# Kernel tuning notes

Measured on AMD Instinct MI355X. Metric: run time of the kernel, lower is better.

Reference implementation:

```python
import jax, jax.numpy as jnp
import numpy as np

N_NODES = 100000
N_EDGES = 800000
NODE_F = 32
EDGE_F = 16
HID = 128
EPS = 1e-5


def _bn(h, g, b):
    # BatchNorm1d in training mode: biased batch stats over dim 0
    m = h.mean(axis=0)
    v = jnp.mean((h - m) ** 2, axis=0)
    return (h - m) * jax.lax.rsqrt(v + EPS) * g + b


def _sage(x, src, dst, Wl, bl, Wr):
    # PyG SAGEConv (mean aggr): lin_l(mean_{j->i} x_j) + lin_r(x_i)
    s = jax.ops.segment_sum(x[src], dst, num_segments=N_NODES)
    cnt = jax.ops.segment_sum(jnp.ones((src.shape[0], 1), x.dtype), dst, num_segments=N_NODES)
    mean = s / jnp.maximum(cnt, 1.0)
    return mean @ Wl + bl + x @ Wr


def setup_inputs() -> dict:
    key = jax.random.key(0)
    ks = jax.random.split(key, 32)

    def lin(k, fi, fo):
        return jax.random.normal(k, (fi, fo), jnp.float32) / np.sqrt(fi)

    inp = {
        'x': jax.random.normal(ks[0], (N_NODES, NODE_F), jnp.float32),
        'edge_index': jax.random.randint(ks[1], (2, N_EDGES), 0, N_NODES),
        'edge_attr': jax.random.normal(ks[2], (N_EDGES, EDGE_F), jnp.float32),
        'edge_source': jax.random.randint(ks[3], (N_EDGES,), 0, N_NODES),
        'edge_target': jax.random.randint(ks[4], (N_EDGES,), 0, N_NODES),
        'W1l': lin(ks[5], NODE_F, HID), 'b1': jnp.zeros((HID,), jnp.float32), 'W1r': lin(ks[6], NODE_F, HID),
        'W2l': lin(ks[7], HID, HID), 'b2': jnp.zeros((HID,), jnp.float32), 'W2r': lin(ks[8], HID, HID),
        'bn1_g': jnp.ones((HID,), jnp.float32), 'bn1_b': jnp.zeros((HID,), jnp.float32),
        'bn2_g': jnp.ones((HID,), jnp.float32), 'bn2_b': jnp.zeros((HID,), jnp.float32),
        'We': lin(ks[9], EDGE_F, HID), 'be': jnp.zeros((HID,), jnp.float32),
        'bne_g': jnp.ones((HID,), jnp.float32), 'bne_b': jnp.zeros((HID,), jnp.float32),
        'Wm1': lin(ks[10], 3 * HID, HID), 'bm1': jnp.zeros((HID,), jnp.float32),
        'bnm_g': jnp.ones((HID,), jnp.float32), 'bnm_b': jnp.zeros((HID,), jnp.float32),
        'Wm2': lin(ks[11], HID, HID // 2), 'bm2': jnp.zeros((HID // 2,), jnp.float32),
        'Wm3': lin(ks[12], HID // 2, 1), 'bm3': jnp.zeros((1,), jnp.float32),
    }
    return inp


def reference(x, edge_index, edge_attr, edge_source, edge_target,
              W1l, b1, W1r, W2l, b2, W2r, bn1_g, bn1_b, bn2_g, bn2_b,
              We, be, bne_g, bne_b, Wm1, bm1, bnm_g, bnm_b, Wm2, bm2, Wm3, bm3):
    src, dst = edge_index[0], edge_index[1]
    h = jax.nn.relu(_bn(_sage(x, src, dst, W1l, b1, W1r), bn1_g, bn1_b))  # dropout = identity (eval)
    h = jax.nn.relu(_bn(_sage(h, src, dst, W2l, b2, W2r), bn2_g, bn2_b))
    ef = _bn(jax.nn.relu(edge_attr @ We + be), bne_g, bne_b)  # Linear->ReLU->BN->Dropout(id)
    z = jnp.concatenate([h[edge_source], h[edge_target], ef], axis=1)  # [E, 3*HID]
    z = _bn(jax.nn.relu(z @ Wm1 + bm1), bnm_g, bnm_b)
    z = jax.nn.relu(z @ Wm2 + bm2)
    return (z @ Wm3 + bm3).squeeze(-1)
```

## Files before the change

kernel.cpp:

```cpp
#include <hip/hip_runtime.h>
#include <hip/hip_bf16.h>

#define NN 100000
#define NE 800000
#define SCAN_NB 98

typedef __attribute__((ext_vector_type(8))) short bf16x8;
typedef __attribute__((ext_vector_type(4))) float f32x4;

__device__ __forceinline__ short f2b(float f) {
    unsigned u = __float_as_uint(f);
    unsigned r = (u + 0x7fffu + ((u >> 16) & 1u)) >> 16;
    return (short)r;
}
__device__ __forceinline__ float b2f(short s) {
    return __uint_as_float(((unsigned)(unsigned short)s) << 16);
}

__global__ __launch_bounds__(256) void k_hist(const int* __restrict__ ei, int* __restrict__ deg)
{
    int e = blockIdx.x * 256 + threadIdx.x;
    if (e < NE) atomicAdd(&deg[ei[NE + e]], 1);
}

__global__ __launch_bounds__(1024) void k_scan_a(const int* __restrict__ deg,
    int* __restrict__ tmp, int* __restrict__ bsum)
{
    __shared__ int sh[1024];
    int t = threadIdx.x, b = blockIdx.x;
    int idx = b * 1024 + t;
    int v = (idx < NN) ? deg[idx] : 0;
    sh[t] = v;
    __syncthreads();
    for (int ofs = 1; ofs < 1024; ofs <<= 1) {
        int u = (t >= ofs) ? sh[t - ofs] : 0;
        __syncthreads();
        sh[t] += u;
        __syncthreads();
    }
    if (idx < NN) tmp[idx] = sh[t] - v;
    if (t == 1023) bsum[b] = sh[1023];
}

__global__ void k_scan_b(const int* __restrict__ bsum, int* __restrict__ boff,
    int* __restrict__ rowptr)
{
    if (threadIdx.x == 0) {
        int acc = 0;
        for (int i = 0; i < SCAN_NB; i++) { boff[i] = acc; acc += bsum[i]; }
        rowptr[NN] = acc;
    }
}

__global__ __launch_bounds__(1024) void k_scan_c(const int* __restrict__ tmp,
    const int* __restrict__ boff, int* __restrict__ rowptr, int* __restrict__ wp)
{
    int b = blockIdx.x, t = threadIdx.x;
    int idx = b * 1024 + t;
    if (idx < NN) {
        int v = boff[b] + tmp[idx];
        rowptr[idx] = v; wp[idx] = v;
    }
}

__global__ __launch_bounds__(256) void k_scatter(const int* __restrict__ ei,
    int* __restrict__ wp, int* __restrict__ elist)
{
    int e = blockIdx.x * 256 + threadIdx.x;
    if (e < NE) {
        int d = ei[NE + e];
        int pos = atomicAdd(&wp[d], 1);
        elist[pos] = ei[e];
    }
}

__global__ __launch_bounds__(256) void k_gagg1(const float* __restrict__ x,
    const int* __restrict__ rowptr, const int* __restrict__ elist, float* __restrict__ meanX)
{
    int n = blockIdx.x * 8 + (threadIdx.x >> 5);
    int j = threadIdx.x & 31;
    int b = rowptr[n], e = rowptr[n + 1];
    float acc = 0.f;
    for (int i = b; i < e; i++) {
        int s = elist[i];
        acc += x[(size_t)s * 32 + j];
    }
    float inv = (e > b) ? 1.0f / (float)(e - b) : 1.0f;
    meanX[(size_t)n * 32 + j] = acc * inv;
}

__global__ __launch_bounds__(256) void k_gagg2(const short* __restrict__ h1b,
    const int* __restrict__ rowptr, const int* __restrict__ elist,
    const float* __restrict__ sc1, const float* __restrict__ sh1, short* __restrict__ m2b)
{
    int n = blockIdx.x * 8 + (threadIdx.x >> 5);
    int c0 = (threadIdx.x & 31) * 4;
    float sc[4], sh[4];
    #pragma unroll
    for (int i = 0; i < 4; i++) { sc[i] = sc1[c0 + i]; sh[i] = sh1[c0 + i]; }
    int b = rowptr[n], e = rowptr[n + 1];
    float acc[4] = {0.f, 0.f, 0.f, 0.f};
    for (int i = b; i < e; i++) {
        int s = elist[i];
        ushort4 u = *(const ushort4*)(h1b + (size_t)s * 128 + c0);
        acc[0] += fmaxf(b2f((short)u.x) * sc[0] + sh[0], 0.f);
        acc[1] += fmaxf(b2f((short)u.y) * sc[1] + sh[1], 0.f);
        acc[2] += fmaxf(b2f((short)u.z) * sc[2] + sh[2], 0.f);
        acc[3] += fmaxf(b2f((short)u.w) * sc[3] + sh[3], 0.f);
    }
    float inv = (e > b) ? 1.0f / (float)(e - b) : 1.0f;
    ushort4 o;
    o.x = (unsigned short)f2b(acc[0] * inv);
    o.y = (unsigned short)f2b(acc[1] * inv);
    o.z = (unsigned short)f2b(acc[2] * inv);
    o.w = (unsigned short)f2b(acc[3] * inv);
    *(ushort4*)(m2b + (size_t)n * 128 + c0) = o;
}

__global__ __launch_bounds__(256) void k_node_l1(
    const float* __restrict__ meanX, const float* __restrict__ x,
    const float* __restrict__ Wl, const float* __restrict__ Wr,
    const float* __restrict__ bias,
    short* __restrict__ outp, float* __restrict__ ssum, float* __restrict__ ssq)
{
    __shared__ __align__(16) float sWl[32][128];
    __shared__ __align__(16) float sWr[32][128];
    __shared__ __align__(16) float sA[32][36];
    __shared__ __align__(16) float sB[32][36];
    __shared__ float red[2][128], red2[2][128];
    int tid = threadIdx.x;
    int j = tid & 127, rg = tid >> 7;
    int r0 = blockIdx.x * 32;

    for (int f = tid * 4; f < 4096; f += 1024) {
        *(float4*)((float*)sWl + f) = *(const float4*)(Wl + f);
        *(float4*)((float*)sWr + f) = *(const float4*)(Wr + f);
    }
    {
        int r = tid >> 3, c = (tid & 7) * 4;
        *(float4*)(&sA[r][c]) = *(const float4*)(meanX + (size_t)(r0 + r) * 32 + c);
        *(float4*)(&sB[r][c]) = *(const float4*)(x + (size_t)(r0 + r) * 32 + c);
    }
    __syncthreads();

    float acc[16];
    #pragma unroll
    for (int r = 0; r < 16; r++) acc[r] = 0.0f;
    int rb = rg * 16;
    #pragma unroll
    for (int kq = 0; kq < 8; kq++) {
        int k = kq * 4;
        float wl0 = sWl[k][j], wl1 = sWl[k+1][j], wl2 = sWl[k+2][j], wl3 = sWl[k+3][j];
        float wr0 = sWr[k][j], wr1 = sWr[k+1][j], wr2 = sWr[k+2][j], wr3 = sWr[k+3][j];
        #pragma unroll
        for (int r = 0; r < 16; r++) {
            float4 a = *(float4*)(&sA[rb + r][k]);
            float4 b = *(float4*)(&sB[rb + r][k]);
            acc[r] += a.x*wl0 + a.y*wl1 + a.z*wl2 + a.w*wl3
                    + b.x*wr0 + b.y*wr1 + b.z*wr2 + b.w*wr3;
        }
    }
    float bj = bias[j];
    float s1 = 0.0f, s2 = 0.0f;
    #pragma unroll
    for (int r = 0; r < 16; r++) {
        float v = acc[r] + bj;
        outp[(size_t)(r0 + rb + r) * 128 + j] = f2b(v);
        s1 += v; s2 += v * v;
    }
    red[rg][j] = s1; red2[rg][j] = s2;
    __syncthreads();
    if (rg == 0) {
        atomicAdd(&ssum[j], red[0][j] + red[1][j]);
        atomicAdd(&ssq[j],  red2[0][j] + red2[1][j]);
    }
}

__global__ __launch_bounds__(256) void k_node_l2m(
    const short* __restrict__ m2b, const short* __restrict__ h1b,
    const float* __restrict__ sc1, const float* __restrict__ sh1,
    const short* __restrict__ W2cT, const float* __restrict__ bias,
    short* __restrict__ h2b, float* __restrict__ ssum, float* __restrict__ ssq)
{
    __shared__ __align__(16) short sK[32][264];
    __shared__ float sRed[2][128];
    __shared__ float sS[128], sH[128];
    const int tid = threadIdx.x;
    const int wave = tid >> 6, lane = tid & 63, quad = lane >> 4, ln = lane & 15;
    const int waveM = wave >> 1, waveN = wave & 1;
    const int colbase = 64 * waveN, row16 = 16 * waveM;
    if (tid < 128) { sS[tid] = sc1[tid]; sH[tid] = sh1[tid]; sRed[0][tid] = 0.f; sRed[1][tid] = 0.f; }

    bf16x8 bW[4][8];
    #pragma unroll
    for (int nt = 0; nt < 4; nt++)
        #pragma unroll
        for (int kk = 0; kk < 8; kk++)
            bW[nt][kk] = *(const bf16x8*)(W2cT + (size_t)(colbase + nt * 16 + ln) * 256 + kk * 32 + quad * 8);
    float bc[4];
    #pragma unroll
    for (int nt = 0; nt < 4; nt++) bc[nt] = bias[colbase + nt * 16 + ln];

    float s1[4] = {0,0,0,0}, s2[4] = {0,0,0,0};
    f32x4 zero = {0.f, 0.f, 0.f, 0.f};
    __syncthreads();

    for (int t = blockIdx.x; t < NN / 32; t += gridDim.x) {
        int r0 = t * 32;
        __syncthreads();
        {
            int r = tid >> 3, seg = tid & 7;
            if (seg < 4) {
                const bf16x8* src = (const bf16x8*)(m2b + (size_t)(r0 + r) * 128 + seg * 32);
                bf16x8* dst = (bf16x8*)(&sK[r][seg * 32]);
                dst[0] = src[0]; dst[1] = src[1]; dst[2] = src[2]; dst[3] = src[3];
            } else {
                int c0 = (seg - 4) * 32;
                const short* src = h1b + (size_t)(r0 + r) * 128 + c0;
                short tmp[32];
                #pragma unroll
                for (int i = 0; i < 32; i++)
                    tmp[i] = f2b(fmaxf(b2f(src[i]) * sS[c0 + i] + sH[c0 + i], 0.f));
                bf16x8* dst = (bf16x8*)(&sK[r][128 + c0]);
                dst[0] = *(bf16x8*)(tmp); dst[1] = *(bf16x8*)(tmp + 8);
                dst[2] = *(bf16x8*)(tmp + 16); dst[3] = *(bf16x8*)(tmp + 24);
            }
        }
        __syncthreads();
        f32x4 acc[4] = {zero, zero, zero, zero};
        #pragma unroll
        for (int kk = 0; kk < 8; kk++) {
            bf16x8 a = *(const bf16x8*)(&sK[row16 + ln][kk * 32 + quad * 8]);
            #pragma unroll
            for (int nt = 0; nt < 4; nt++)
                acc[nt] = __builtin_amdgcn_mfma_f32_16x16x32_bf16(a, bW[nt][kk], acc[nt], 0, 0, 0);
        }
        #pragma unroll
        for (int nt = 0; nt < 4; nt++) {
            int col = colbase + nt * 16 + ln;
            #pragma unroll
            for (int r = 0; r < 4; r++) {
                float v = acc[nt][r] + bc[nt];
                h2b[(size_t)(r0 + row16 + quad * 4 + r) * 128 + col] = f2b(v);
                s1[nt] += v; s2[nt] += v * v;
            }
        }
    }
    #pragma unroll
    for (int nt = 0; nt < 4; nt++) {
        float a1 = s1[nt], a2 = s2[nt];
        a1 += __shfl_down(a1, 32); a1 += __shfl_down(a1, 16);
        a2 += __shfl_down(a2, 32); a2 += __shfl_down(a2, 16);
        if (quad == 0) {
            atomicAdd(&sRed[0][colbase + nt * 16 + ln], a1);
            atomicAdd(&sRed[1][colbase + nt * 16 + ln], a2);
        }
    }
    __syncthreads();
    if (tid < 128) {
        atomicAdd(&ssum[tid], sRed[0][tid]);
        atomicAdd(&ssq[tid],  sRed[1][tid]);
    }
}

__global__ void k_bn_fin(const float* __restrict__ ssum, const float* __restrict__ ssq,
    const float* __restrict__ g, const float* __restrict__ b, float count,
    float* __restrict__ scale, float* __restrict__ shift)
{
    int j = threadIdx.x;
    float m = ssum[j] / count;
    float var = ssq[j] / count - m * m;
    float rs = rsqrtf(var + 1e-5f);
    float sc = g[j] * rs;
    scale[j] = sc;
    shift[j] = b[j] - m * sc;
}

__global__ void k_prep(const float* __restrict__ We, const float* __restrict__ Wm1,
                       const float* __restrict__ W2l, const float* __restrict__ W2r,
                       short* __restrict__ WteT, short* __restrict__ WmsT,
                       short* __restrict__ WmdT, short* __restrict__ W2cT)
{
    int j = threadIdx.x;
    int b = blockIdx.x;
    if (b == 0) {
        for (int k = 0; k < 32; k++)
            WteT[j * 32 + k] = (k < 16) ? f2b(We[k * 128 + j]) : (short)0;
    } else if (b == 1) {
        for (int k = 0; k < 128; k++) WmsT[j * 128 + k] = f2b(Wm1[k * 128 + j]);
    } else if (b == 2) {
        for (int k = 0; k < 128; k++) WmdT[j * 128 + k] = f2b(Wm1[(128 + k) * 128 + j]);
    } else if (b == 3) {
        for (int k = 0; k < 128; k++) W2cT[j * 256 + k] = f2b(W2l[k * 128 + j]);
    } else {
        for (int k = 0; k < 128; k++) W2cT[j * 256 + 128 + k] = f2b(W2r[k * 128 + j]);
    }
}

__global__ void k_fold_e(const float* __restrict__ ssum, const float* __restrict__ ssq,
    const float* __restrict__ g, const float* __restrict__ b,
    const float* __restrict__ Wm1, const float* __restrict__ bm1,
    short* __restrict__ W1pT, float* __restrict__ bm1p)
{
    __shared__ float sa[128], sc[128];
    int tid = threadIdx.x;
    float m = ssum[tid] / (float)NE;
    float var = ssq[tid] / (float)NE - m * m;
    float rs = rsqrtf(var + 1e-5f);
    float a = g[tid] * rs;
    sa[tid] = a; sc[tid] = b[tid] - m * a;
    __syncthreads();
    float acc = bm1[tid];
    for (int k = 0; k < 128; k++) {
        float w = Wm1[(256 + k) * 128 + tid];
        W1pT[tid * 128 + k] = f2b(sa[k] * w);
        acc += sc[k] * w;
    }
    bm1p[tid] = acc;
}

__global__ void k_fold_m(const float* __restrict__ ssum, const float* __restrict__ ssq,
    const float* __restrict__ g, const float* __restrict__ b,
    const float* __restrict__ Wm2, const float* __restrict__ bm2,
    short* __restrict__ W2pT, float* __restrict__ b2p)
{
    __shared__ float sa[128], sc[128];
    int tid = threadIdx.x;
    float m = ssum[tid] / (float)NE;
    float var = ssq[tid] / (float)NE - m * m;
    float rs = rsqrtf(var + 1e-5f);
    float a = g[tid] * rs;
    sa[tid] = a; sc[tid] = b[tid] - m * a;
    __syncthreads();
    if (tid < 64) {
        float acc = bm2[tid];
        for (int k = 0; k < 128; k++) {
            float w = Wm2[k * 64 + tid];
            W2pT[tid * 128 + k] = f2b(sa[k] * w);
            acc += sc[k] * w;
        }
        b2p[tid] = acc;
    }
}

__global__ __launch_bounds__(256) void k_proj_mfma(
    const short* __restrict__ h2b, const float* __restrict__ sc2, const float* __restrict__ sh2,
    const short* __restrict__ WT, short* __restrict__ C)
{
    __shared__ __align__(16) short sA[32][136];
    __shared__ float sS[128], sH[128];
    const int tid = threadIdx.x;
    const int wave = tid >> 6, lane = tid & 63, quad = lane >> 4, ln = lane & 15;
    const int waveM = wave >> 1, waveN = wave & 1;
    const int colbase = 64 * waveN, row16 = 16 * waveM;
    if (tid < 128) { sS[tid] = sc2[tid]; sH[tid] = sh2[tid]; }
    bf16x8 bW[4][4];
    #pragma unroll
    for (int nt = 0; nt < 4; nt++)
        #pragma unroll
        for (int kk = 0; kk < 4; kk++)
            bW[nt][kk] = *(const bf16x8*)(WT + (colbase + nt * 16 + ln) * 128 + kk * 32 + quad * 8);
    f32x4 zero = {0.f, 0.f, 0.f, 0.f};
    __syncthreads();
    for (int t = blockIdx.x; t < NN / 32; t += gridDim.x) {
        int r0 = t * 32;
        __syncthreads();
        {
            int r = tid >> 3, c0 = (tid & 7) * 16;
            const short* p = h2b + (size_t)(r0 + r) * 128 + c0;
            short tmp[16];
            #pragma unroll
            for (int i = 0; i < 16; i++)
                tmp[i] = f2b(fmaxf(b2f(p[i]) * sS[c0 + i] + sH[c0 + i], 0.f));
            *(bf16x8*)(&sA[r][c0])     = *(bf16x8*)tmp;
            *(bf16x8*)(&sA[r][c0 + 8]) = *(bf16x8*)(tmp + 8);
        }
        __syncthreads();
        f32x4 acc[4] = {zero, zero, zero, zero};
        #pragma unroll
        for (int kk = 0; kk < 4; kk++) {
            bf16x8 a = *(const bf16x8*)(&sA[row16 + ln][kk * 32 + quad * 8]);
            #pragma unroll
            for (int nt = 0; nt < 4; nt++)
                acc[nt] = __builtin_amdgcn_mfma_f32_16x16x32_bf16(a, bW[nt][kk], acc[nt], 0, 0, 0);
        }
        #pragma unroll
        for (int nt = 0; nt < 4; nt++) {
            int col = colbase + nt * 16 + ln;
            #pragma unroll
            for (int r = 0; r < 4; r++)
                C[(size_t)(r0 + row16 + quad * 4 + r) * 128 + col] = f2b(acc[nt][r]);
        }
    }
}

template<int MODE, bool STOREV = false>
__global__ __launch_bounds__(256) void k_edge_mfma(
    const float* __restrict__ ea,
    const short* __restrict__ WteT, const float* __restrict__ be,
    const short* __restrict__ W1pT, const float* __restrict__ bm1p,
    const short* __restrict__ hs, const short* __restrict__ hd,
    const int* __restrict__ esrc, const int* __restrict__ etgt,
    const short* __restrict__ W2pT, const float* __restrict__ b2p,
    const float* __restrict__ Wm3, const float* __restrict__ bm3,
    float* __restrict__ ssum, float* __restrict__ ssq,
    short* __restrict__ vbuf, float* __restrict__ outp)
{
    __shared__ __align__(16) short sT[32][136];
    __shared__ float sRed[2][128];
    __shared__ __align__(16) short sW2[64][136];
    __shared__ float sZ[32][69];
    __shared__ float sW3[64];

    const int tid = threadIdx.x;
    const int wave = tid >> 6, lane = tid & 63;
    const int quad = lane >> 4, ln = lane & 15;
    const int waveM = wave >> 1, waveN = wave & 1;
    const int colbase = 64 * waveN, row16 = 16 * waveM;

    if (MODE < 2) {
        if (tid < 128) { sRed[0][tid] = 0.f; sRed[1][tid] = 0.f; }
    }
    if (MODE >= 2) {
        int q = tid >> 2, kb = (tid & 3) * 32;
        const bf16x8* src = (const bf16x8*)(W2pT + q * 128 + kb);
        bf16x8* dst = (bf16x8*)(&sW2[q][kb]);
        dst[0] = src[0]; dst[1] = src[1]; dst[2] = src[2]; dst[3] = src[3];
        if (tid < 64) sW3[tid] = Wm3[tid];
    }

    bf16x8 bWe[4], bW1[4][4];
    if (MODE <= 2) {
        #pragma unroll
        for (int nt = 0; nt < 4; nt++) {
            bWe[nt] = *(const bf16x8*)(WteT + (colbase + nt * 16 + ln) * 32 + quad * 8);
            if (MODE >= 1) {
                #pragma unroll
                for (int kk = 0; kk < 4; kk++)
                    bW1[nt][kk] = *(const bf16x8*)(W1pT + (colbase + nt * 16 + ln) * 128 + kk * 32 + quad * 8);
            }
        }
    }
    float bec[4], bmc[4];
    #pragma unroll
    for (int nt = 0; nt < 4; nt++) {
        bec[nt] = (MODE <= 2) ? be[colbase + nt * 16 + ln] : 0.f;
        bmc[nt] = (MODE == 1 || MODE == 2) ? bm1p[colbase + nt * 16 + ln] : 0.f;
    }
    float b2c[2] = {0.f, 0.f};
    if (MODE >= 2) { b2c[0] = b2p[32 * waveN + ln]; b2c[1] = b2p[32 * waveN + 16 + ln]; }
    float bm3v = (MODE >= 2) ? bm3[0] : 0.f;

    float s1[4] = {0,0,0,0}, s2[4] = {0,0,0,0};
    f32x4 zero = {0.f, 0.f, 0.f, 0.f};
    __syncthreads();

    for (int t = blockIdx.x; t < NE / 32; t += gridDim.x) {
        const int e0 = t * 32;

        if (MODE == 3) {
            f32x4 vacc[2] = {zero, zero};
            #pragma unroll
            for (int kk = 0; kk < 4; kk++) {
                bf16x8 aV = *(const bf16x8*)(vbuf + (size_t)(e0 + row16 + ln) * 128 + kk * 32 + quad * 8);
                #pragma unroll
                for (int n2 = 0; n2 < 2; n2++) {
                    bf16x8 bV = *(const bf16x8*)(&sW2[32 * waveN + n2 * 16 + ln][kk * 32 + quad * 8]);
                    vacc[n2] = __builtin_amdgcn_mfma_f32_16x16x32_bf16(aV, bV, vacc[n2], 0, 0, 0);
                }
            }
            __syncthreads();
            #pragma unroll
            for (int n2 = 0; n2 < 2; n2++) {
                int col2 = 32 * waveN + n2 * 16 + ln;
                #pragma unroll
                for (int r = 0; r < 4; r++)
                    sZ[row16 + quad * 4 + r][col2] = fmaxf(vacc[n2][r] + b2c[n2], 0.f);
            }
            __syncthreads();
            if (wave == 0) {
                int rw = lane & 31, half = lane >> 5;
                float o = 0.f;
                #pragma unroll 8
                for (int k2 = 0; k2 < 32; k2++)
                    o += sZ[rw][half * 32 + k2] * sW3[half * 32 + k2];
                o += __shfl_down(o, 32);
                if (lane < 32) outp[e0 + rw] = o + bm3v;
            }
            continue;
        }

        bf16x8 aE;
        #pragma unroll
        for (int i = 0; i < 8; i++) aE[i] = 0;
        if (quad < 2) {
            const float* p = ea + (size_t)(e0 + row16 + ln) * 16 + quad * 8;
            float4 f0 = *(const float4*)p, f1 = *(const float4*)(p + 4);
            aE[0]=f2b(f0.x); aE[1]=f2b(f0.y); aE[2]=f2b(f0.z); aE[3]=f2b(f0.w);
            aE[4]=f2b(f1.x); aE[5]=f2b(f1.y); aE[6]=f2b(f1.z); aE[7]=f2b(f1.w);
        }
        f32x4 tacc[4];
        #pragma unroll
        for (int nt = 0; nt < 4; nt++)
            tacc[nt] = __builtin_amdgcn_mfma_f32_16x16x32_bf16(aE, bWe[nt], zero, 0, 0, 0);

        if (MODE == 0) {
            #pragma unroll
            for (int nt = 0; nt < 4; nt++)
                #pragma unroll
                for (int r = 0; r < 4; r++) {
                    float v = fmaxf(tacc[nt][r] + bec[nt], 0.f);
                    s1[nt] += v; s2[nt] += v * v;
                }
            continue;
        }

        __syncthreads();
        #pragma unroll
        for (int nt = 0; nt < 4; nt++) {
            int col = colbase + nt * 16 + ln;
            #pragma unroll
            for (int r = 0; r < 4; r++)
                sT[row16 + quad * 4 + r][col] = f2b(fmaxf(tacc[nt][r] + bec[nt], 0.f));
        }
        __syncthreads();

        f32x4 uacc[4] = {zero, zero, zero, zero};
        #pragma unroll
        for (int kk = 0; kk < 4; kk++) {
            bf16x8 aU = *(const bf16x8*)(&sT[row16 + ln][kk * 32 + quad * 8]);
            #pragma unroll
            for (int nt = 0; nt < 4; nt++)
                uacc[nt] = __builtin_amdgcn_mfma_f32_16x16x32_bf16(aU, bW1[nt][kk], uacc[nt], 0, 0, 0);
        }

        int4 is4 = *(const int4*)(esrc + e0 + row16 + quad * 4);
        int4 it4 = *(const int4*)(etgt + e0 + row16 + quad * 4);
        int isv[4] = {is4.x, is4.y, is4.z, is4.w};
        int itv[4] = {it4.x, it4.y, it4.z, it4.w};

        if (MODE == 1) {
            #pragma unroll
            for (int nt = 0; nt < 4; nt++) {
                int col = colbase + nt * 16 + ln;
                #pragma unroll
                for (int r = 0; r < 4; r++) {
                    float v = uacc[nt][r] + bmc[nt]
                            + b2f(hs[(size_t)isv[r] * 128 + col]) + b2f(hd[(size_t)itv[r] * 128 + col]);
                    v = fmaxf(v, 0.f);
                    s1[nt] += v; s2[nt] += v * v;
                    if constexpr (STOREV)
                        vbuf[(size_t)(e0 + row16 + quad * 4 + r) * 128 + col] = f2b(v);
                }
            }
        } else {
            __syncthreads();
            #pragma unroll
            for (int nt = 0; nt < 4; nt++) {
                int col = colbase + nt * 16 + ln;
                #pragma unroll
                for (int r = 0; r < 4; r++) {
                    float v = uacc[nt][r] + bmc[nt]
                            + b2f(hs[(size_t)isv[r] * 128 + col]) + b2f(hd[(size_t)itv[r] * 128 + col]);
                    sT[row16 + quad * 4 + r][col] = f2b(fmaxf(v, 0.f));
                }
            }
            __syncthreads();
            f32x4 vacc[2] = {zero, zero};
            #pragma unroll
            for (int kk = 0; kk < 4; kk++) {
                bf16x8 aV = *(const bf16x8*)(&sT[row16 + ln][kk * 32 + quad * 8]);
                #pragma unroll
                for (int n2 = 0; n2 < 2; n2++) {
                    bf16x8 bV = *(const bf16x8*)(&sW2[32 * waveN + n2 * 16 + ln][kk * 32 + quad * 8]);
                    vacc[n2] = __builtin_amdgcn_mfma_f32_16x16x32_bf16(aV, bV, vacc[n2], 0, 0, 0);
                }
            }
            #pragma unroll
            for (int n2 = 0; n2 < 2; n2++) {
                int col2 = 32 * waveN + n2 * 16 + ln;
                #pragma unroll
                for (int r = 0; r < 4; r++)
                    sZ[row16 + quad * 4 + r][col2] = fmaxf(vacc[n2][r] + b2c[n2], 0.f);
            }
            __syncthreads();
            if (wave == 0) {
                int rw = lane & 31, half = lane >> 5;
                float o = 0.f;
                #pragma unroll 8
                for (int k2 = 0; k2 < 32; k2++)
                    o += sZ[rw][half * 32 + k2] * sW3[half * 32 + k2];
                o += __shfl_down(o, 32);
                if (lane < 32) outp[e0 + rw] = o + bm3v;
            }
        }
    }

    if (MODE < 2) {
        #pragma unroll
        for (int nt = 0; nt < 4; nt++) {
            float a1 = s1[nt], a2 = s2[nt];
            a1 += __shfl_down(a1, 32); a1 += __shfl_down(a1, 16);
            a2 += __shfl_down(a2, 32); a2 += __shfl_down(a2, 16);
            if (quad == 0) {
                atomicAdd(&sRed[0][colbase + nt * 16 + ln], a1);
                atomicAdd(&sRed[1][colbase + nt * 16 + ln], a2);
            }
        }
        __syncthreads();
        if (tid < 128) {
            atomicAdd(&ssum[tid], sRed[0][tid]);
            atomicAdd(&ssq[tid],  sRed[1][tid]);
        }
    }
}

extern "C" void kernel_launch(void* const* d_in, const int* in_sizes, int n_in,
                              void* d_out, int out_size, void* d_ws, size_t ws_size,
                              hipStream_t stream) {
    const float* x     = (const float*)d_in[0];
    const int*   ei    = (const int*)  d_in[1];
    const float* eattr = (const float*)d_in[2];
    const int*   esrc  = (const int*)  d_in[3];
    const int*   etgt  = (const int*)  d_in[4];
    const float* W1l = (const float*)d_in[5];  const float* b1 = (const float*)d_in[6];
    const float* W1r = (const float*)d_in[7];
    const float* W2l = (const float*)d_in[8];  const float* b2 = (const float*)d_in[9];
    const float* W2r = (const float*)d_in[10];
    const float* bn1_g = (const float*)d_in[11]; const float* bn1_b = (const float*)d_in[12];
    const float* bn2_g = (const float*)d_in[13]; const float* bn2_b = (const float*)d_in[14];
    const float* We  = (const float*)d_in[15]; const float* be  = (const float*)d_in[16];
    const float* bne_g = (const float*)d_in[17]; const float* bne_b = (const float*)d_in[18];
    const float* Wm1 = (const float*)d_in[19]; const float* bm1 = (const float*)d_in[20];
    const float* bnm_g = (const float*)d_in[21]; const float* bnm_b = (const float*)d_in[22];
    const float* Wm2 = (const float*)d_in[23]; const float* bm2 = (const float*)d_in[24];
    const float* Wm3 = (const float*)d_in[25]; const float* bm3 = (const float*)d_in[26];
    float* out = (float*)d_out;

    char* base = (char*)d_ws;
    size_t o = 0;
    auto A = [&](size_t bytes) { char* p = base + o; o = (o + bytes + 255) & ~(size_t)255; return p; };
    short* hsb   = (short*)A((size_t)NN * 128 * 2);
    short* hdb   = (short*)A((size_t)NN * 128 * 2);
    int*   deg   = (int*)  A((size_t)NN * 4);
    int*   rowptr= (int*)  A((size_t)(NN + 1) * 4);
    int*   wp    = (int*)  A((size_t)NN * 4);
    int*   elist = (int*)  A((size_t)NE * 4);
    float* st    = (float*)A(1024 * 4);
    int*   bsum  = (int*)  A(SCAN_NB * 4);
    int*   boff  = (int*)  A(SCAN_NB * 4);
    float* sc1   = (float*)A(512); float* sh1 = (float*)A(512);
    float* sc2   = (float*)A(512); float* sh2 = (float*)A(512);
    float* bm1p  = (float*)A(512); float* b2p = (float*)A(256);
    short* WteT  = (short*)A(128 * 32 * 2);
    short* W1pT  = (short*)A(128 * 128 * 2);
    short* WmsT  = (short*)A(128 * 128 * 2);
    short* WmdT  = (short*)A(128 * 128 * 2);
    short* W2pT  = (short*)A(64 * 128 * 2);
    short* W2cT  = (short*)A(128 * 256 * 2);
    size_t chain = o;
    float* meanX = (float*)A((size_t)NN * 32 * 4);
    short* h1b   = (short*)A((size_t)NN * 128 * 2);
    short* m2b   = (short*)A((size_t)NN * 128 * 2);
    short* h2b   = (short*)A((size_t)NN * 128 * 2);
    int*   stmp  = (int*)meanX;
    short* vbuf  = (short*)(base + chain);
    bool storev = ws_size >= chain + (size_t)NE * 128 * 2;

    hipMemsetAsync(deg, 0, (size_t)NN * 4, stream);
    hipMemsetAsync(st, 0, 1024 * 4, stream);

    k_prep<<<5, 128, 0, stream>>>(We, Wm1, W2l, W2r, WteT, WmsT, WmdT, W2cT);
    k_hist<<<(NE + 255) / 256, 256, 0, stream>>>(ei, deg);
    k_scan_a<<<SCAN_NB, 1024, 0, stream>>>(deg, stmp, bsum);
    k_scan_b<<<1, 64, 0, stream>>>(bsum, boff, rowptr);
    k_scan_c<<<SCAN_NB, 1024, 0, stream>>>(stmp, boff, rowptr, wp);
    k_scatter<<<(NE + 255) / 256, 256, 0, stream>>>(ei, wp, elist);

    k_edge_mfma<0><<<1024, 256, 0, stream>>>(eattr, WteT, be, W1pT, bm1p, hsb, hdb,
        esrc, etgt, W2pT, b2p, Wm3, bm3, st + 512, st + 640, nullptr, out);
    k_fold_e<<<1, 128, 0, stream>>>(st + 512, st + 640, bne_g, bne_b, Wm1, bm1, W1pT, bm1p);

    k_gagg1<<<NN / 8, 256, 0, stream>>>(x, rowptr, elist, meanX);
    k_node_l1<<<NN / 32, 256, 0, stream>>>(meanX, x, W1l, W1r, b1, h1b, st + 0, st + 128);
    k_bn_fin<<<1, 128, 0, stream>>>(st + 0, st + 128, bn1_g, bn1_b, (float)NN, sc1, sh1);

    k_gagg2<<<NN / 8, 256, 0, stream>>>(h1b, rowptr, elist, sc1, sh1, m2b);
    k_node_l2m<<<640, 256, 0, stream>>>(m2b, h1b, sc1, sh1, W2cT, b2, h2b, st + 256, st + 384);
    k_bn_fin<<<1, 128, 0, stream>>>(st + 256, st + 384, bn2_g, bn2_b, (float)NN, sc2, sh2);

    k_proj_mfma<<<640, 256, 0, stream>>>(h2b, sc2, sh2, WmsT, hsb);
    k_proj_mfma<<<640, 256, 0, stream>>>(h2b, sc2, sh2, WmdT, hdb);

    if (storev)
        k_edge_mfma<1, true><<<1280, 256, 0, stream>>>(eattr, WteT, be, W1pT, bm1p, hsb, hdb,
            esrc, etgt, W2pT, b2p, Wm3, bm3, st + 768, st + 896, vbuf, out);
    else
        k_edge_mfma<1, false><<<1280, 256, 0, stream>>>(eattr, WteT, be, W1pT, bm1p, hsb, hdb,
            esrc, etgt, W2pT, b2p, Wm3, bm3, st + 768, st + 896, nullptr, out);
    k_fold_m<<<1, 128, 0, stream>>>(st + 768, st + 896, bnm_g, bnm_b, Wm2, bm2, W2pT, b2p);

    if (storev)
        k_edge_mfma<3><<<2048, 256, 0, stream>>>(eattr, WteT, be, W1pT, bm1p, hsb, hdb,
            esrc, etgt, W2pT, b2p, Wm3, bm3, nullptr, nullptr, vbuf, out);
    else
        k_edge_mfma<2><<<1280, 256, 0, stream>>>(eattr, WteT, be, W1pT, bm1p, hsb, hdb,
            esrc, etgt, W2pT, b2p, Wm3, bm3, nullptr, nullptr, nullptr, out);
}
```

Measured before the change: 864.4 us.

## Coalesce edge gathers via shared staging, merge proj launches, parallelize final dot

Edge kernels now gather the hs[src] and hd[tgt] rows with 16-byte vector loads per thread, issued before the MFMA. The summed values are staged in a new shared fp32 tile, replacing scattered per-element bf16 gathers in the epilogue. The two projection launches are merged into one 1280-block launch, and the final 64-wide dot product is spread across all four waves with xor shuffles instead of one wave. Launch bounds request 5 blocks per CU, which may pressure registers, and the added shared tile raises LDS use per block.

```diff
diff --git a/kernel.cpp b/kernel.cpp
--- a/kernel.cpp
+++ b/kernel.cpp
@@ -345,7 +345,8 @@
 
 __global__ __launch_bounds__(256) void k_proj_mfma(
     const short* __restrict__ h2b, const float* __restrict__ sc2, const float* __restrict__ sh2,
-    const short* __restrict__ WT, short* __restrict__ C)
+    const short* __restrict__ WT0, const short* __restrict__ WT1,
+    short* __restrict__ C0, short* __restrict__ C1)
 {
     __shared__ __align__(16) short sA[32][136];
     __shared__ float sS[128], sH[128];
@@ -353,6 +354,10 @@
     const int wave = tid >> 6, lane = tid & 63, quad = lane >> 4, ln = lane & 15;
     const int waveM = wave >> 1, waveN = wave & 1;
     const int colbase = 64 * waveN, row16 = 16 * waveM;
+    const int half = (blockIdx.x >= 640) ? 1 : 0;
+    const short* WT = half ? WT1 : WT0;
+    short* C = half ? C1 : C0;
+    const int b0 = blockIdx.x - half * 640;
     if (tid < 128) { sS[tid] = sc2[tid]; sH[tid] = sh2[tid]; }
     bf16x8 bW[4][4];
     #pragma unroll
@@ -362,7 +367,7 @@
             bW[nt][kk] = *(const bf16x8*)(WT + (colbase + nt * 16 + ln) * 128 + kk * 32 + quad * 8);
     f32x4 zero = {0.f, 0.f, 0.f, 0.f};
     __syncthreads();
-    for (int t = blockIdx.x; t < NN / 32; t += gridDim.x) {
+    for (int t = b0; t < NN / 32; t += 640) {
         int r0 = t * 32;
         __syncthreads();
         {
@@ -395,7 +400,7 @@
 }
 
 template<int MODE, bool STOREV = false>
-__global__ __launch_bounds__(256) void k_edge_mfma(
+__global__ __launch_bounds__(256, 5) void k_edge_mfma(
     const float* __restrict__ ea,
     const short* __restrict__ WteT, const float* __restrict__ be,
     const short* __restrict__ W1pT, const float* __restrict__ bm1p,
@@ -407,6 +412,7 @@
     short* __restrict__ vbuf, float* __restrict__ outp)
 {
     __shared__ __align__(16) short sT[32][136];
+    __shared__ __align__(16) float sSum[32][132];
     __shared__ float sRed[2][128];
     __shared__ __align__(16) short sW2[64][136];
     __shared__ float sZ[32][69];
@@ -451,6 +457,9 @@
     if (MODE >= 2) { b2c[0] = b2p[32 * waveN + ln]; b2c[1] = b2p[32 * waveN + 16 + ln]; }
     float bm3v = (MODE >= 2) ? bm3[0] : 0.f;
 
+    const int srow = tid >> 4;
+    const int scol = (tid & 15) * 8;
+
     float s1[4] = {0,0,0,0}, s2[4] = {0,0,0,0};
     f32x4 zero = {0.f, 0.f, 0.f, 0.f};
     __syncthreads();
@@ -478,16 +487,25 @@
                     sZ[row16 + quad * 4 + r][col2] = fmaxf(vacc[n2][r] + b2c[n2], 0.f);
             }
             __syncthreads();
-            if (wave == 0) {
-                int rw = lane & 31, half = lane >> 5;
+            {
+                int row = wave * 8 + (lane >> 3);
+                int ks  = (lane & 7) * 8;
                 float o = 0.f;
-                #pragma unroll 8
-                for (int k2 = 0; k2 < 32; k2++)
-                    o += sZ[rw][half * 32 + k2] * sW3[half * 32 + k2];
-                o += __shfl_down(o, 32);
-                if (lane < 32) outp[e0 + rw] = o + bm3v;
+                #pragma unroll
+                for (int k2 = 0; k2 < 8; k2++)
+                    o += sZ[row][ks + k2] * sW3[ks + k2];
+                o += __shfl_xor(o, 1);
+                o += __shfl_xor(o, 2);
+                o += __shfl_xor(o, 4);
+                if ((lane & 7) == 0) outp[e0 + row] = o + bm3v;
             }
             continue;
+        }
+
+        int isA = 0, itA = 0, isB = 0, itB = 0;
+        if (MODE >= 1) {
+            isA = esrc[e0 + srow];      itA = etgt[e0 + srow];
+            isB = esrc[e0 + srow + 16]; itB = etgt[e0 + srow + 16];
         }
 
         bf16x8 aE;
@@ -516,12 +534,30 @@
         }
 
         __syncthreads();
-        #pragma unroll
-        for (int nt = 0; nt < 4; nt++) {
-            int col = colbase + nt * 16 + ln;
-            #pragma unroll
-            for (int r = 0; r < 4; r++)
-                sT[row16 + quad * 4 + r][col] = f2b(fmaxf(tacc[nt][r] + bec[nt], 0.f));
+        {
+            bf16x8 gA = *(const bf16x8*)(hs + (size_t)isA * 128 + scol);
+            bf16x8 gB = *(const bf16x8*)(hd + (size_t)itA * 128 + scol);
+            bf16x8 gC = *(const bf16x8*)(hs + (size_t)isB * 128 + scol);
+            bf16x8 gD = *(const bf16x8*)(hd + (size_t)itB * 128 + scol);
+            #pragma unroll
+            for (int nt = 0; nt < 4; nt++) {
+                int col = colbase + nt * 16 + ln;
+                #pragma unroll
+                for (int r = 0; r < 4; r++)
+                    sT[row16 + quad * 4 + r][col] = f2b(fmaxf(tacc[nt][r] + bec[nt], 0.f));
+            }
+            f32x4 a0, a1, b0, b1;
+            #pragma unroll
+            for (int i = 0; i < 4; i++) {
+                a0[i] = b2f(gA[i])     + b2f(gB[i]);
+                a1[i] = b2f(gA[i + 4]) + b2f(gB[i + 4]);
+                b0[i] = b2f(gC[i])     + b2f(gD[i]);
+                b1[i] = b2f(gC[i + 4]) + b2f(gD[i + 4]);
+            }
+            *(f32x4*)(&sSum[srow][scol])          = a0;
+            *(f32x4*)(&sSum[srow][scol + 4])      = a1;
+            *(f32x4*)(&sSum[srow + 16][scol])     = b0;
+            *(f32x4*)(&sSum[srow + 16][scol + 4]) = b1;
         }
         __syncthreads();
 
@@ -534,19 +570,13 @@
                 uacc[nt] = __builtin_amdgcn_mfma_f32_16x16x32_bf16(aU, bW1[nt][kk], uacc[nt], 0, 0, 0);
         }
 
-        int4 is4 = *(const int4*)(esrc + e0 + row16 + quad * 4);
-        int4 it4 = *(const int4*)(etgt + e0 + row16 + quad * 4);
-        int isv[4] = {is4.x, is4.y, is4.z, is4.w};
-        int itv[4] = {it4.x, it4.y, it4.z, it4.w};
-
         if (MODE == 1) {
             #pragma unroll
             for (int nt = 0; nt < 4; nt++) {
                 int col = colbase + nt * 16 + ln;
                 #pragma unroll
                 for (int r = 0; r < 4; r++) {
-                    float v = uacc[nt][r] + bmc[nt]
-                            + b2f(hs[(size_t)isv[r] * 128 + col]) + b2f(hd[(size_t)itv[r] * 128 + col]);
+                    float v = uacc[nt][r] + bmc[nt] + sSum[row16 + quad * 4 + r][col];
                     v = fmaxf(v, 0.f);
                     s1[nt] += v; s2[nt] += v * v;
                     if constexpr (STOREV)
@@ -560,8 +590,7 @@
                 int col = colbase + nt * 16 + ln;
                 #pragma unroll
                 for (int r = 0; r < 4; r++) {
-                    float v = uacc[nt][r] + bmc[nt]
-                            + b2f(hs[(size_t)isv[r] * 128 + col]) + b2f(hd[(size_t)itv[r] * 128 + col]);
+                    float v = uacc[nt][r] + bmc[nt] + sSum[row16 + quad * 4 + r][col];
                     sT[row16 + quad * 4 + r][col] = f2b(fmaxf(v, 0.f));
                 }
             }
@@ -584,14 +613,17 @@
                     sZ[row16 + quad * 4 + r][col2] = fmaxf(vacc[n2][r] + b2c[n2], 0.f);
             }
             __syncthreads();
-            if (wave == 0) {
-                int rw = lane & 31, half = lane >> 5;
+            {
+                int row = wave * 8 + (lane >> 3);
+                int ks  = (lane & 7) * 8;
                 float o = 0.f;
-                #pragma unroll 8
-                for (int k2 = 0; k2 < 32; k2++)
-                    o += sZ[rw][half * 32 + k2] * sW3[half * 32 + k2];
-                o += __shfl_down(o, 32);
-                if (lane < 32) outp[e0 + rw] = o + bm3v;
+                #pragma unroll
+                for (int k2 = 0; k2 < 8; k2++)
+                    o += sZ[row][ks + k2] * sW3[ks + k2];
+                o += __shfl_xor(o, 1);
+                o += __shfl_xor(o, 2);
+                o += __shfl_xor(o, 4);
+                if ((lane & 7) == 0) outp[e0 + row] = o + bm3v;
             }
         }
     }
@@ -689,8 +721,7 @@
     k_node_l2m<<<640, 256, 0, stream>>>(m2b, h1b, sc1, sh1, W2cT, b2, h2b, st + 256, st + 384);
     k_bn_fin<<<1, 128, 0, stream>>>(st + 256, st + 384, bn2_g, bn2_b, (float)NN, sc2, sh2);
 
-    k_proj_mfma<<<640, 256, 0, stream>>>(h2b, sc2, sh2, WmsT, hsb);
-    k_proj_mfma<<<640, 256, 0, stream>>>(h2b, sc2, sh2, WmdT, hdb);
+    k_proj_mfma<<<1280, 256, 0, stream>>>(h2b, sc2, sh2, WmsT, WmdT, hsb, hdb);
 
     if (storev)
         k_edge_mfma<1, true><<<1280, 256, 0, stream>>>(eattr, WteT, be, W1pT, bm1p, hsb, hdb,
```

New measurement: 996.1 us. 1.15x slower.
